# Performance work log

Measured on AMD Instinct MI355X. Metric: run time of the kernel, lower is better.

The kernel has to match this reference:

```python
import jax, jax.numpy as jnp
import numpy as np

N, D_IN, D_HID, D_OUT = 200000, 512, 2048, 1


def _mlp(x, W1, b1, W2, b2):
    # 2-layer MLP: Linear -> ReLU -> Linear
    h = jax.nn.relu(x @ W1.T + b1)  # [N, hidden]
    return h @ W2.T + b2            # [N, out]


def setup_inputs() -> dict:
    key = jax.random.key(0)
    ks = jax.random.split(key, 14)
    s1 = 1.0 / np.sqrt(D_IN)
    s2 = 1.0 / np.sqrt(D_HID)
    x = jax.random.normal(ks[0], (N, D_IN), dtype=jnp.float32)
    atomic_nums = jax.random.randint(ks[1], (N,), 0, 10, dtype=jnp.int64)
    def lin(k, fan_out, fan_in, s):
        return jax.random.uniform(k, (fan_out, fan_in), jnp.float32, -s, s)
    inp = {"x": x, "atomic_nums": atomic_nums}
    names = ["c", "h", "o"]
    for i, n in enumerate(names):
        inp[n + "W1"] = lin(ks[2 + 4 * i], D_HID, D_IN, s1)
        inp[n + "b1"] = jax.random.uniform(ks[3 + 4 * i], (D_HID,), jnp.float32, -s1, s1)
        inp[n + "W2"] = lin(ks[4 + 4 * i], D_OUT, D_HID, s2)
        inp[n + "b2"] = jax.random.uniform(ks[5 + 4 * i], (D_OUT,), jnp.float32, -s2, s2)
    return inp


def reference(x, atomic_nums, cW1, cb1, cW2, cb2, hW1, hb1, hW2, hb2, oW1, ob1, oW2, ob2):
    mask_c = (atomic_nums == 6)[:, None]  # carbon
    mask_h = (atomic_nums == 1)[:, None]  # hydrogen
    out_c = _mlp(x, cW1, cb1, cW2, cb2)
    out_h = _mlp(x, hW1, hb1, hW2, hb2)
    out_o = _mlp(x, oW1, ob1, oW2, ob2)
    # hard routing: carbon -> carbon_mlp, hydrogen -> hydrogen_mlp, else other_mlp
    return jnp.where(mask_c, out_c, jnp.where(mask_h, out_h, out_o))
```

## Files before the change

kernel.cpp:

```cpp
#include <hip/hip_runtime.h>

#define N_ROWS 200000
#define D_IN   512
#define D_HID  2048
#define BM     128
#define NBLK   ((N_ROWS + BM - 1) / BM)
#define JT     16
#define NJT    (D_HID / JT)

typedef short  bf16x8 __attribute__((ext_vector_type(8)));
typedef float  f32x4  __attribute__((ext_vector_type(4)));
typedef unsigned short u16x4 __attribute__((ext_vector_type(4)));

#define CNT_OFS  0
#define PERM_OFS 16
#define W1_OFS   (PERM_OFS + 3 * N_ROWS * 4)

__device__ __forceinline__ unsigned short f2bf(float f) {
  unsigned u = __builtin_bit_cast(unsigned, f);
  u += 0x7fffu + ((u >> 16) & 1u);
  return (unsigned short)(u >> 16);
}

__global__ void k_convert(const float* __restrict__ w1c, const float* __restrict__ w1h,
                          const float* __restrict__ w1o, unsigned short* __restrict__ dst) {
  const int per = (D_HID * D_IN) / 4;
  int i = blockIdx.x * 256 + threadIdx.x;
  if (i >= 3 * per) return;
  int t = i / per, r = i - t * per;
  const float* src = (t == 0) ? w1c : ((t == 1) ? w1h : w1o);
  f32x4 v = *(const f32x4*)(src + r * 4);
  u16x4 o;
  o[0] = f2bf(v[0]); o[1] = f2bf(v[1]); o[2] = f2bf(v[2]); o[3] = f2bf(v[3]);
  *(u16x4*)(dst + (size_t)i * 4) = o;
}

__global__ void k_route(const int* __restrict__ an, int* __restrict__ cnt,
                        int* __restrict__ perm) {
  int i = blockIdx.x * 256 + threadIdx.x;
  int lane = threadIdx.x & 63;
  int t = -1;
  if (i < N_ROWS) {
    int a = an[i];
    t = (a == 6) ? 0 : ((a == 1) ? 1 : 2);
  }
#pragma unroll
  for (int tt = 0; tt < 3; ++tt) {
    unsigned long long m = __ballot(t == tt);
    if (t == tt) {
      int off = (int)__popcll(m & ((1ull << lane) - 1ull));
      int base = 0;
      if (off == 0) base = atomicAdd(&cnt[tt], (int)__popcll(m));
      base = __shfl(base, (int)(__ffsll((long long)m) - 1), 64);
      perm[tt * N_ROWS + base + off] = i;
    }
  }
}

__global__ __launch_bounds__(256, 2) void k_mlp(
    const float* __restrict__ x,
    const unsigned short* __restrict__ w1base,
    const int* __restrict__ perm, const int* __restrict__ cnt,
    const float* __restrict__ b1c, const float* __restrict__ b1h, const float* __restrict__ b1o,
    const float* __restrict__ w2c, const float* __restrict__ w2h, const float* __restrict__ w2o,
    const float* __restrict__ b2c, const float* __restrict__ b2h, const float* __restrict__ b2o,
    float* __restrict__ out) {
  int bid = blockIdx.x;
  int t = bid / NBLK, m = bid - t * NBLK;
  int cnt_t = cnt[t];
  int base_row = m * BM;
  if (base_row >= cnt_t) return;

  const unsigned short* w1 = w1base + (size_t)t * (D_HID * D_IN);
  const float* b1 = (t == 0) ? b1c : ((t == 1) ? b1h : b1o);
  const float* w2 = (t == 0) ? w2c : ((t == 1) ? w2h : w2o);
  const float* b2 = (t == 0) ? b2c : ((t == 1) ? b2h : b2o);
  const int* permt = perm + t * N_ROWS;

  const int tid = threadIdx.x;
  const int w = tid >> 6, lane = tid & 63;
  const int lj = lane & 15, lq = lane >> 4;

  __shared__ __align__(16) unsigned short smem[2 * JT * D_IN];

  int rowg[2];
#pragma unroll
  for (int rf = 0; rf < 2; ++rf) {
    int idx = base_row + w * 32 + rf * 16 + lj;
    idx = min(idx, cnt_t - 1);
    rowg[rf] = permt[idx];
  }
  bf16x8 afrag[2][16];
#pragma unroll
  for (int rf = 0; rf < 2; ++rf) {
    const float* xr = x + (size_t)rowg[rf] * D_IN + lq * 8;
#pragma unroll
    for (int ks = 0; ks < 16; ++ks) {
      f32x4 v0 = *(const f32x4*)(xr + ks * 32);
      f32x4 v1 = *(const f32x4*)(xr + ks * 32 + 4);
      bf16x8 a;
      a[0] = (short)f2bf(v0[0]); a[1] = (short)f2bf(v0[1]);
      a[2] = (short)f2bf(v0[2]); a[3] = (short)f2bf(v0[3]);
      a[4] = (short)f2bf(v1[0]); a[5] = (short)f2bf(v1[1]);
      a[6] = (short)f2bf(v1[2]); a[7] = (short)f2bf(v1[3]);
      afrag[rf][ks] = a;
    }
  }

  auto stage = [&](int buf, int j0) {
#pragma unroll
    for (int c = 0; c < 4; ++c) {
      int r = w * 4 + c;
      const unsigned short* src = w1 + (size_t)(j0 + r) * D_IN + ((lane ^ (r & 7)) * 8);
      unsigned short* dst = &smem[buf * (JT * D_IN) + r * D_IN];
      __builtin_amdgcn_global_load_lds(
          (const __attribute__((address_space(1))) unsigned int*)src,
          (__attribute__((address_space(3))) unsigned int*)dst, 16, 0, 0);
    }
  };

  stage(0, 0);
  f32x4 osum0 = {0.f, 0.f, 0.f, 0.f}, osum1 = {0.f, 0.f, 0.f, 0.f};
  const int chunk0 = lq ^ (lj & 7);
  const unsigned short* bbase = &smem[lj * D_IN];
  __syncthreads();

  for (int jt = 0; jt < NJT; ++jt) {
    int cur = jt & 1;
    if (jt + 1 < NJT) stage(cur ^ 1, (jt + 1) * JT);
    float b1v = b1[jt * JT + lj];
    float w2v = w2[jt * JT + lj];
    f32x4 acc0 = {0.f, 0.f, 0.f, 0.f}, acc1 = {0.f, 0.f, 0.f, 0.f};
    const unsigned short* bb = bbase + cur * (JT * D_IN);
#pragma unroll
    for (int ks = 0; ks < 16; ++ks) {
      bf16x8 bfrag = *(const bf16x8*)(bb + ((((ks << 2) ^ chunk0)) << 3));
      acc0 = __builtin_amdgcn_mfma_f32_16x16x32_bf16(afrag[0][ks], bfrag, acc0, 0, 0, 0);
      acc1 = __builtin_amdgcn_mfma_f32_16x16x32_bf16(afrag[1][ks], bfrag, acc1, 0, 0, 0);
    }
#pragma unroll
    for (int q = 0; q < 4; ++q) {
      osum0[q] += fmaxf(acc0[q] + b1v, 0.f) * w2v;
      osum1[q] += fmaxf(acc1[q] + b1v, 0.f) * w2v;
    }
    __syncthreads();
  }

  float b2v = b2[0];
#pragma unroll
  for (int rf = 0; rf < 2; ++rf) {
    f32x4 os = rf ? osum1 : osum0;
#pragma unroll
    for (int q = 0; q < 4; ++q) {
      float v = os[q];
      v += __shfl_xor(v, 1, 64);
      v += __shfl_xor(v, 2, 64);
      v += __shfl_xor(v, 4, 64);
      v += __shfl_xor(v, 8, 64);
      int idx = base_row + w * 32 + rf * 16 + lq * 4 + q;
      if (lj == 0 && idx < cnt_t) out[permt[idx]] = v + b2v;
    }
  }
}

extern "C" void kernel_launch(void* const* d_in, const int* in_sizes, int n_in,
                              void* d_out, int out_size, void* d_ws, size_t ws_size,
                              hipStream_t stream) {
  const float* x  = (const float*)d_in[0];
  const int* an   = (const int*)d_in[1];
  const float* w1c = (const float*)d_in[2],  *b1c = (const float*)d_in[3];
  const float* w2c = (const float*)d_in[4],  *b2c = (const float*)d_in[5];
  const float* w1h = (const float*)d_in[6],  *b1h = (const float*)d_in[7];
  const float* w2h = (const float*)d_in[8],  *b2h = (const float*)d_in[9];
  const float* w1o = (const float*)d_in[10], *b1o = (const float*)d_in[11];
  const float* w2o = (const float*)d_in[12], *b2o = (const float*)d_in[13];
  float* out = (float*)d_out;

  int* cnt  = (int*)d_ws;
  int* perm = (int*)((char*)d_ws + PERM_OFS);
  unsigned short* w1bf = (unsigned short*)((char*)d_ws + W1_OFS);

  hipMemsetAsync(d_ws, 0, 16, stream);
  k_convert<<<(3 * (D_HID * D_IN) / 4 + 255) / 256, 256, 0, stream>>>(w1c, w1h, w1o, w1bf);
  k_route<<<(N_ROWS + 255) / 256, 256, 0, stream>>>(an, cnt, perm);
  k_mlp<<<3 * NBLK, 256, 0, stream>>>(x, w1bf, perm, cnt,
                                      b1c, b1h, b1o, w2c, w2h, w2o,
                                      b2c, b2h, b2o, out);
}
```

Measured before the change: 1.077 ms.

## Stable scan-based routing, MFMA-ordered W1 LDS layout, prefetch biases, raise occupancy

Replaces the atomic-based routing with a count/scan/scatter pipeline, so the row permutation is deterministic and keeps input order within each type. The W1 tile is staged into LDS in an order that matches the MFMA fragment layout, replacing the XOR swizzle with contiguous reads. Next-tile bias and W2 values are prefetched, the MFMA loop runs with raised wave priority, and launch bounds move from 2 to 3 blocks per CU. This adds two more kernel launches and a single-block scan, and the tighter register budget risks spilling the large A-fragment array.

```diff
diff --git a/kernel.cpp b/kernel.cpp
--- a/kernel.cpp
+++ b/kernel.cpp
@@ -7,14 +7,17 @@
 #define NBLK   ((N_ROWS + BM - 1) / BM)
 #define JT     16
 #define NJT    (D_HID / JT)
+#define NCB    ((N_ROWS + 255) / 256)
 
 typedef short  bf16x8 __attribute__((ext_vector_type(8)));
 typedef float  f32x4  __attribute__((ext_vector_type(4)));
 typedef unsigned short u16x4 __attribute__((ext_vector_type(4)));
 
 #define CNT_OFS  0
-#define PERM_OFS 16
-#define W1_OFS   (PERM_OFS + 3 * N_ROWS * 4)
+#define BC_OFS   16
+#define BASE_OFS (BC_OFS + NCB * 16)
+#define PERM_OFS (BASE_OFS + NCB * 16)
+#define W1_OFS   (((PERM_OFS + 3 * N_ROWS * 4) + 15) & ~15)
 
 __device__ __forceinline__ unsigned short f2bf(float f) {
   unsigned u = __builtin_bit_cast(unsigned, f);
@@ -35,29 +38,73 @@
   *(u16x4*)(dst + (size_t)i * 4) = o;
 }
 
-__global__ void k_route(const int* __restrict__ an, int* __restrict__ cnt,
-                        int* __restrict__ perm) {
-  int i = blockIdx.x * 256 + threadIdx.x;
-  int lane = threadIdx.x & 63;
+__global__ void k_count(const int* __restrict__ an, int* __restrict__ bc) {
+  int b = blockIdx.x;
+  int i = b * 256 + threadIdx.x;
+  int lane = threadIdx.x & 63, w = threadIdx.x >> 6;
   int t = -1;
-  if (i < N_ROWS) {
-    int a = an[i];
-    t = (a == 6) ? 0 : ((a == 1) ? 1 : 2);
-  }
+  if (i < N_ROWS) { int a = an[i]; t = (a == 6) ? 0 : ((a == 1) ? 1 : 2); }
+  __shared__ int wc[4][3];
 #pragma unroll
   for (int tt = 0; tt < 3; ++tt) {
     unsigned long long m = __ballot(t == tt);
-    if (t == tt) {
-      int off = (int)__popcll(m & ((1ull << lane) - 1ull));
-      int base = 0;
-      if (off == 0) base = atomicAdd(&cnt[tt], (int)__popcll(m));
-      base = __shfl(base, (int)(__ffsll((long long)m) - 1), 64);
-      perm[tt * N_ROWS + base + off] = i;
-    }
-  }
-}
-
-__global__ __launch_bounds__(256, 2) void k_mlp(
+    if (lane == 0) wc[w][tt] = (int)__popcll(m);
+  }
+  __syncthreads();
+  if (threadIdx.x < 3) {
+    int tt = threadIdx.x;
+    bc[b * 4 + tt] = wc[0][tt] + wc[1][tt] + wc[2][tt] + wc[3][tt];
+  }
+}
+
+__global__ void k_scan(const int* __restrict__ bc, int* __restrict__ bases,
+                       int* __restrict__ cnt) {
+  __shared__ int s[1024];
+  int i = threadIdx.x;
+  for (int t = 0; t < 3; ++t) {
+    int v = (i < NCB) ? bc[i * 4 + t] : 0;
+    int x = v;
+    s[i] = x;
+    __syncthreads();
+    for (int off = 1; off < 1024; off <<= 1) {
+      int a = (i >= off) ? s[i - off] : 0;
+      __syncthreads();
+      x += a;
+      s[i] = x;
+      __syncthreads();
+    }
+    if (i < NCB) bases[i * 4 + t] = x - v;
+    if (i == 0) cnt[t] = s[1023];
+    __syncthreads();
+  }
+}
+
+__global__ void k_scatter(const int* __restrict__ an, const int* __restrict__ bases,
+                          int* __restrict__ perm) {
+  int b = blockIdx.x;
+  int i = b * 256 + threadIdx.x;
+  int lane = threadIdx.x & 63, w = threadIdx.x >> 6;
+  int t = -1;
+  if (i < N_ROWS) { int a = an[i]; t = (a == 6) ? 0 : ((a == 1) ? 1 : 2); }
+  __shared__ int wc[4][3];
+  unsigned long long mm[3];
+#pragma unroll
+  for (int tt = 0; tt < 3; ++tt) {
+    mm[tt] = __ballot(t == tt);
+    if (lane == 0) wc[w][tt] = (int)__popcll(mm[tt]);
+  }
+  __syncthreads();
+  if (t >= 0) {
+    unsigned long long m = mm[t];
+    int off = (int)__popcll(m & ((1ull << lane) - 1ull));
+    int pre = 0;
+#pragma unroll
+    for (int ww = 0; ww < 3; ++ww) if (ww < w) pre += wc[ww][t];
+    perm[t * N_ROWS + bases[b * 4 + t] + pre + off] = i;
+  }
+}
+
+__global__ __launch_bounds__(256, 3) void k_mlp(
     const float* __restrict__ x,
     const unsigned short* __restrict__ w1base,
     const int* __restrict__ perm, const int* __restrict__ cnt,
@@ -110,9 +157,10 @@
   auto stage = [&](int buf, int j0) {
 #pragma unroll
     for (int c = 0; c < 4; ++c) {
-      int r = w * 4 + c;
-      const unsigned short* src = w1 + (size_t)(j0 + r) * D_IN + ((lane ^ (r & 7)) * 8);
-      unsigned short* dst = &smem[buf * (JT * D_IN) + r * D_IN];
+      int g = w * 4 + c;
+      const unsigned short* src =
+          w1 + (size_t)(j0 + (lane >> 2)) * D_IN + (g * 4 + (lane & 3)) * 8;
+      unsigned short* dst = &smem[buf * (JT * D_IN) + g * 512];
       __builtin_amdgcn_global_load_lds(
           (const __attribute__((address_space(1))) unsigned int*)src,
           (__attribute__((address_space(3))) unsigned int*)dst, 16, 0, 0);
@@ -121,28 +169,31 @@
 
   stage(0, 0);
   f32x4 osum0 = {0.f, 0.f, 0.f, 0.f}, osum1 = {0.f, 0.f, 0.f, 0.f};
-  const int chunk0 = lq ^ (lj & 7);
-  const unsigned short* bbase = &smem[lj * D_IN];
+  const unsigned short* bbase = &smem[(lj * 4 + lq) * 8];
+  float b1v = b1[lj], w2v = w2[lj];
   __syncthreads();
 
   for (int jt = 0; jt < NJT; ++jt) {
     int cur = jt & 1;
     if (jt + 1 < NJT) stage(cur ^ 1, (jt + 1) * JT);
-    float b1v = b1[jt * JT + lj];
-    float w2v = w2[jt * JT + lj];
+    float b1n = 0.f, w2n = 0.f;
+    if (jt + 1 < NJT) { b1n = b1[(jt + 1) * JT + lj]; w2n = w2[(jt + 1) * JT + lj]; }
     f32x4 acc0 = {0.f, 0.f, 0.f, 0.f}, acc1 = {0.f, 0.f, 0.f, 0.f};
     const unsigned short* bb = bbase + cur * (JT * D_IN);
+    __builtin_amdgcn_s_setprio(1);
 #pragma unroll
     for (int ks = 0; ks < 16; ++ks) {
-      bf16x8 bfrag = *(const bf16x8*)(bb + ((((ks << 2) ^ chunk0)) << 3));
+      bf16x8 bfrag = *(const bf16x8*)(bb + ks * 512);
       acc0 = __builtin_amdgcn_mfma_f32_16x16x32_bf16(afrag[0][ks], bfrag, acc0, 0, 0, 0);
       acc1 = __builtin_amdgcn_mfma_f32_16x16x32_bf16(afrag[1][ks], bfrag, acc1, 0, 0, 0);
     }
+    __builtin_amdgcn_s_setprio(0);
 #pragma unroll
     for (int q = 0; q < 4; ++q) {
-      osum0[q] += fmaxf(acc0[q] + b1v, 0.f) * w2v;
-      osum1[q] += fmaxf(acc1[q] + b1v, 0.f) * w2v;
-    }
+      osum0[q] = fmaf(fmaxf(acc0[q] + b1v, 0.f), w2v, osum0[q]);
+      osum1[q] = fmaf(fmaxf(acc1[q] + b1v, 0.f), w2v, osum1[q]);
+    }
+    b1v = b1n; w2v = w2n;
     __syncthreads();
   }
 
@@ -176,13 +227,16 @@
   const float* w2o = (const float*)d_in[12], *b2o = (const float*)d_in[13];
   float* out = (float*)d_out;
 
-  int* cnt  = (int*)d_ws;
-  int* perm = (int*)((char*)d_ws + PERM_OFS);
+  int* cnt   = (int*)((char*)d_ws + CNT_OFS);
+  int* bc    = (int*)((char*)d_ws + BC_OFS);
+  int* bases = (int*)((char*)d_ws + BASE_OFS);
+  int* perm  = (int*)((char*)d_ws + PERM_OFS);
   unsigned short* w1bf = (unsigned short*)((char*)d_ws + W1_OFS);
 
-  hipMemsetAsync(d_ws, 0, 16, stream);
   k_convert<<<(3 * (D_HID * D_IN) / 4 + 255) / 256, 256, 0, stream>>>(w1c, w1h, w1o, w1bf);
-  k_route<<<(N_ROWS + 255) / 256, 256, 0, stream>>>(an, cnt, perm);
+  k_count<<<NCB, 256, 0, stream>>>(an, bc);
+  k_scan<<<1, 1024, 0, stream>>>(bc, bases, cnt);
+  k_scatter<<<NCB, 256, 0, stream>>>(an, bases, perm);
   k_mlp<<<3 * NBLK, 256, 0, stream>>>(x, w1bf, perm, cnt,
                                       b1c, b1h, b1o, w2c, w2h, w2o,
                                       b2c, b2h, b2o, out);
```

Result: slower. 2.720 ms (+152.4%).
